# Performance work log

Measured on AMD Instinct MI355X. Metric: run time of the kernel, lower is better.

The kernel has to match this reference:

```python
import jax, jax.numpy as jnp
import numpy as np

TEXTURE_W, SHAPE_W, INTENSITY_W = 1.0, 0.5, 1.0
EPS = 1e-08


def _conv2d_same(x, k):
    # x: [B,1,H,W], k: [1,1,3,3], zero padding 1 (SAME)
    return jax.lax.conv_general_dilated(
        x, k, window_strides=(1, 1), padding='SAME',
        dimension_numbers=('NCHW', 'OIHW', 'NCHW'))


def _box_mean(x):
    # mean over 3x3 zero-padded window == F.unfold(k=3,pad=1).mean(dim=1) for C=1
    k = jnp.ones((1, 1, 3, 3), x.dtype) / 9.0
    return _conv2d_same(x, k)


def _local_variance(x):
    # mean((patch - patch_mean)^2) == E[x^2] - E[x]^2 over the padded 3x3 window
    m = _box_mean(x)
    m2 = _box_mean(x * x)
    return m2 - m * m


def _intensity_loss(inp, out, mask):
    ms = mask.sum() + EPS
    im = (inp * mask).sum() / ms
    om = (out * mask).sum() / ms
    di, do = inp - im, out - om
    iv = (di * di * mask).sum() / ms
    ov = (do * do * mask).sum() / ms
    isk = (di ** 3 * mask).sum() / (ms * (iv ** 1.5 + EPS))
    osk = (do ** 3 * mask).sum() / (ms * (ov ** 1.5 + EPS))
    iku = (di ** 4 * mask).sum() / (ms * (iv ** 2 + EPS))
    oku = (do ** 4 * mask).sum() / (ms * (ov ** 2 + EPS))
    return (im - om) ** 2 + (iv - ov) ** 2 + (isk - osk) ** 2 + (iku - oku) ** 2


def _texture_loss(inp, out, mask):
    it = _local_variance(inp)
    ot = _local_variance(out)
    return jnp.abs(ot * mask - it * mask).mean()


def _shape_loss(inp, out, mask):
    lap = jnp.array([[0., 1., 0.], [1., -4., 1.], [0., 1., 0.]], inp.dtype).reshape(1, 1, 3, 3)
    il = _conv2d_same(inp, lap)
    ol = _conv2d_same(out, lap)
    return jnp.abs(ol * mask - il * mask).mean()


def setup_inputs() -> dict:
    key = jax.random.key(0)
    k1, k2, k3 = jax.random.split(key, 3)
    shape = (32, 1, 512, 512)
    return {
        'input_img': jax.random.normal(k1, shape, jnp.float32),
        'output_img': jax.random.normal(k2, shape, jnp.float32),
        'roi_mask': jax.random.uniform(k3, shape, jnp.float32),
    }


def reference(input_img, output_img, roi_mask):
    intensity = _intensity_loss(input_img, output_img, roi_mask)
    texture = _texture_loss(input_img, output_img, roi_mask)
    shape = _shape_loss(input_img, output_img, roi_mask)
    total = INTENSITY_W * intensity + TEXTURE_W * texture + SHAPE_W * shape
    # stacked [intensity, texture, shape, total] (dict values in original order)
    return jnp.stack([intensity, texture, shape, total])
```

## Files before the change

kernel.cpp:

```cpp
#include <hip/hip_runtime.h>
#include <math.h>

#define H 512
#define W 512
#define BAND 4
#define NQ 11

__device__ __forceinline__ float2 shfl_up1_f2(float2 v, int lane) {
    float2 r;
    r.x = __shfl_up(v.x, 1);
    r.y = __shfl_up(v.y, 1);
    if (lane == 0) { r.x = 0.0f; r.y = 0.0f; }
    return r;
}
__device__ __forceinline__ float2 shfl_dn1_f2(float2 v, int lane) {
    float2 r;
    r.x = __shfl_down(v.x, 1);
    r.y = __shfl_down(v.y, 1);
    if (lane == 63) { r.x = 0.0f; r.y = 0.0f; }
    return r;
}

__device__ __forceinline__ float2 pk_add(float2 a, float2 b) { return make_float2(a.x + b.x, a.y + b.y); }
__device__ __forceinline__ float2 pk_sub(float2 a, float2 b) { return make_float2(a.x - b.x, a.y - b.y); }
__device__ __forceinline__ float2 pk_mul(float2 a, float2 b) { return make_float2(a.x * b.x, a.y * b.y); }
__device__ __forceinline__ float2 pk_muls(float2 a, float s) { return make_float2(a.x * s, a.y * s); }
__device__ __forceinline__ float2 pk_fma(float2 a, float2 b, float2 c) {
    return make_float2(fmaf(a.x, b.x, c.x), fmaf(a.y, b.y, c.y));
}

__device__ __forceinline__ void load_row_pk(const float* __restrict__ inp,
                                            const float* __restrict__ outp,
                                            size_t off, int y, int x0, float2* dst) {
    if (y < 0 || y >= H) {
        #pragma unroll
        for (int j = 0; j < 8; j++) dst[j] = make_float2(0.0f, 0.0f);
    } else {
        const float4* pi = reinterpret_cast<const float4*>(inp  + off + (size_t)y * W + x0);
        const float4* po = reinterpret_cast<const float4*>(outp + off + (size_t)y * W + x0);
        float4 a = pi[0], b = pi[1];
        float4 c = po[0], d = po[1];
        dst[0] = make_float2(a.x, c.x); dst[1] = make_float2(a.y, c.y);
        dst[2] = make_float2(a.z, c.z); dst[3] = make_float2(a.w, c.w);
        dst[4] = make_float2(b.x, d.x); dst[5] = make_float2(b.y, d.y);
        dst[6] = make_float2(b.z, d.z); dst[7] = make_float2(b.w, d.w);
    }
}

__device__ __forceinline__ void load_mask_row(const float* __restrict__ mask, size_t off,
                                              int y, int x0, float* dst) {
    const float4* p = reinterpret_cast<const float4*>(mask + off + (size_t)y * W + x0);
    float4 a = p[0];
    float4 b = p[1];
    dst[0] = a.x; dst[1] = a.y; dst[2] = a.z; dst[3] = a.w;
    dst[4] = b.x; dst[5] = b.y; dst[6] = b.z; dst[7] = b.w;
}

__global__ __launch_bounds__(256) void radiomics_main(
    const float* __restrict__ inp, const float* __restrict__ outp,
    const float* __restrict__ mask, double* __restrict__ partials)
{
    const int tid = threadIdx.x;
    const int lane = tid & 63;
    const int wib = tid >> 6;
    const int gwave = blockIdx.x * 4 + wib;
    const int b = gwave >> 7;
    const int band = gwave & 127;
    const int y0 = band * BAND;
    const size_t off = (size_t)b * H * W;
    const int x0 = lane * 8;

    float2 P[8], C[8], N[8];
    float  Mk[8];

    load_row_pk(inp, outp, off, y0 - 1, x0, P);
    load_row_pk(inp, outp, off, y0,     x0, C);
    load_row_pk(inp, outp, off, y0 + 1, x0, N);
    load_mask_row(mask, off, y0, x0, Mk);

    float  acc0 = 0.0f, accT = 0.0f, accS = 0.0f;
    float2 am1 = make_float2(0,0), am2 = make_float2(0,0);
    float2 am3 = make_float2(0,0), am4 = make_float2(0,0);

    const float inv9 = 1.0f / 9.0f;

    #pragma unroll
    for (int i = 0; i < BAND; i++) {
        if (i) {
            #pragma unroll
            for (int j = 0; j < 8; j++) { P[j] = C[j]; C[j] = N[j]; }
            load_row_pk(inp, outp, off, y0 + i + 1, x0, N);
            load_mask_row(mask, off, y0 + i, x0, Mk);
        }

        float2 s1[8], s2[8];
        #pragma unroll
        for (int j = 0; j < 8; j++) {
            s1[j] = pk_add(pk_add(P[j], C[j]), N[j]);
            s2[j] = pk_fma(P[j], P[j], pk_fma(C[j], C[j], pk_mul(N[j], N[j])));
        }
        float2 h1l = shfl_up1_f2(s1[7], lane), h1r = shfl_dn1_f2(s1[0], lane);
        float2 h2l = shfl_up1_f2(s2[7], lane), h2r = shfl_dn1_f2(s2[0], lane);
        float2 hcl = shfl_up1_f2(C[7],  lane), hcr = shfl_dn1_f2(C[0],  lane);

        #pragma unroll
        for (int j = 0; j < 8; j++) {
            float2 l1 = (j == 0) ? h1l : s1[j-1];
            float2 r1 = (j == 7) ? h1r : s1[j+1];
            float2 l2 = (j == 0) ? h2l : s2[j-1];
            float2 r2 = (j == 7) ? h2r : s2[j+1];
            float2 mn = pk_muls(pk_add(pk_add(l1, s1[j]), r1), inv9);
            float2 e2 = pk_muls(pk_add(pk_add(l2, s2[j]), r2), inv9);
            float2 tv = pk_fma(make_float2(-mn.x, -mn.y), mn, e2);
            float2 cl = (j == 0) ? hcl : C[j-1];
            float2 cr = (j == 7) ? hcr : C[j+1];
            float2 lp = pk_sub(pk_add(pk_add(pk_sub(s1[j], C[j]), cl), cr),
                               pk_muls(C[j], 4.0f));
            float m = Mk[j];
            accT += fabsf(tv.y * m - tv.x * m);
            accS += fabsf(lp.y * m - lp.x * m);
            acc0 += m;
            float2 X = C[j];
            float2 t = pk_muls(X, m);
            am1 = pk_add(am1, t); t = pk_mul(t, X);
            am2 = pk_add(am2, t); t = pk_mul(t, X);
            am3 = pk_add(am3, t); t = pk_mul(t, X);
            am4 = pk_add(am4, t);
        }
    }

    float acc[NQ] = { acc0, am1.x, am2.x, am3.x, am4.x,
                            am1.y, am2.y, am3.y, am4.y, accT, accS };
    #pragma unroll
    for (int q = 0; q < NQ; q++) {
        float v = acc[q];
        #pragma unroll
        for (int o = 32; o > 0; o >>= 1) v += __shfl_down(v, o);
        acc[q] = v;
    }
    __shared__ double red[4][NQ];
    if (lane == 0) {
        #pragma unroll
        for (int q = 0; q < NQ; q++) red[wib][q] = (double)acc[q];
    }
    __syncthreads();
    if (tid < NQ) {
        double s = red[0][tid] + red[1][tid] + red[2][tid] + red[3][tid];
        partials[(size_t)blockIdx.x * NQ + tid] = s;
    }
}

__global__ __launch_bounds__(256) void radiomics_final(
    const double* __restrict__ partials, int nblk, float* __restrict__ out4, double inv_n)
{
    const int tid = threadIdx.x;
    const int lane = tid & 63;
    const int w = tid >> 6;
    double q[NQ];
    #pragma unroll
    for (int k = 0; k < NQ; k++) q[k] = 0.0;
    for (int i = tid; i < nblk; i += 256) {
        #pragma unroll
        for (int k = 0; k < NQ; k++) q[k] += partials[(size_t)i * NQ + k];
    }
    #pragma unroll
    for (int k = 0; k < NQ; k++) {
        #pragma unroll
        for (int o = 32; o > 0; o >>= 1) q[k] += __shfl_down(q[k], o);
    }
    __shared__ double red[4][NQ];
    if (lane == 0) {
        #pragma unroll
        for (int k = 0; k < NQ; k++) red[w][k] = q[k];
    }
    __syncthreads();
    if (tid == 0) {
        double s[NQ];
        #pragma unroll
        for (int k = 0; k < NQ; k++) s[k] = red[0][k] + red[1][k] + red[2][k] + red[3][k];
        const double EPS = 1e-8;
        double S0 = s[0];
        double ms = S0 + EPS;
        double im = s[1] / ms, om = s[5] / ms;
        double im2 = im * im, im3 = im2 * im, im4 = im2 * im2;
        double om2 = om * om, om3 = om2 * om, om4 = om2 * om2;
        double di2 = s[2] - 2.0*im*s[1] + im2*S0;
        double do2 = s[6] - 2.0*om*s[5] + om2*S0;
        double iv = di2 / ms, ov = do2 / ms;
        double di3 = s[3] - 3.0*im*s[2] + 3.0*im2*s[1] - im3*S0;
        double do3 = s[7] - 3.0*om*s[6] + 3.0*om2*s[5] - om3*S0;
        double isk = di3 / (ms * (iv * sqrt(iv) + EPS));
        double osk = do3 / (ms * (ov * sqrt(ov) + EPS));
        double di4 = s[4] - 4.0*im*s[3] + 6.0*im2*s[2] - 4.0*im3*s[1] + im4*S0;
        double do4 = s[8] - 4.0*om*s[7] + 6.0*om2*s[6] - 4.0*om3*s[5] + om4*S0;
        double iku = di4 / (ms * (iv * iv + EPS));
        double oku = do4 / (ms * (ov * ov + EPS));
        double intensity = (im-om)*(im-om) + (iv-ov)*(iv-ov)
                         + (isk-osk)*(isk-osk) + (iku-oku)*(iku-oku);
        double texture = s[9]  * inv_n;
        double shape   = s[10] * inv_n;
        double total = intensity + texture + 0.5 * shape;
        out4[0] = (float)intensity;
        out4[1] = (float)texture;
        out4[2] = (float)shape;
        out4[3] = (float)total;
    }
}

extern "C" void kernel_launch(void* const* d_in, const int* in_sizes, int n_in,
                              void* d_out, int out_size, void* d_ws, size_t ws_size,
                              hipStream_t stream) {
    const float* inp  = (const float*)d_in[0];
    const float* outp = (const float*)d_in[1];
    const float* mask = (const float*)d_in[2];
    const int total = in_sizes[0];
    const int nimg  = total / (H * W);
    const int nwaves = nimg * (H / BAND);
    const int nblk   = nwaves / 4;
    double* partials = (double*)d_ws;

    radiomics_main<<<nblk, 256, 0, stream>>>(inp, outp, mask, partials);
    const double inv_n = 1.0 / (double)total;
    radiomics_final<<<1, 256, 0, stream>>>(partials, nblk, (float*)d_out, inv_n);
}
```

Measured before the change: 124.1 us.

## Fuse final reduction via last-block ticket, double band height, remap blocks across XCDs

Merges the final reduction kernel into the main kernel: each block writes its partials, bumps an atomic ticket, and the last block to finish does the final reduction and writes the four outputs. The band height goes from 4 to 8 rows per wave, which halves the block count and cuts the redundant halo-row loads. Block IDs are remapped so consecutive logical blocks land on the same XCD, aiming for better L2 locality of neighbouring rows. This adds a memset launch for the ticket, a threadfence and an atomic per block, and the tail still has one block doing a serial reduction.

Result: slower. 167.6 us (+35.0%).

```diff
diff --git a/kernel.cpp b/kernel.cpp
--- a/kernel.cpp
+++ b/kernel.cpp
@@ -3,8 +3,9 @@
 
 #define H 512
 #define W 512
-#define BAND 4
+#define BAND 8
 #define NQ 11
+#define CTR_OFF 49152
 
 __device__ __forceinline__ float2 shfl_up1_f2(float2 v, int lane) {
     float2 r;
@@ -56,16 +57,21 @@
     dst[4] = b.x; dst[5] = b.y; dst[6] = b.z; dst[7] = b.w;
 }
 
-__global__ __launch_bounds__(256) void radiomics_main(
+__global__ __launch_bounds__(256) void radiomics_fused(
     const float* __restrict__ inp, const float* __restrict__ outp,
-    const float* __restrict__ mask, double* __restrict__ partials)
+    const float* __restrict__ mask, double* __restrict__ partials,
+    unsigned int* __restrict__ ticket,
+    float* __restrict__ out4, double inv_n, int nblk)
 {
     const int tid = threadIdx.x;
     const int lane = tid & 63;
     const int wib = tid >> 6;
-    const int gwave = blockIdx.x * 4 + wib;
-    const int b = gwave >> 7;
-    const int band = gwave & 127;
+    const int bid = blockIdx.x;
+    const int cpx = nblk >> 3;
+    const int lb = (bid & 7) * cpx + (bid >> 3);
+    const int gwave = lb * 4 + wib;
+    const int b = gwave >> 6;
+    const int band = gwave & 63;
     const int y0 = band * BAND;
     const size_t off = (size_t)b * H * W;
     const int x0 = lane * 8;
@@ -139,6 +145,7 @@
         acc[q] = v;
     }
     __shared__ double red[4][NQ];
+    __shared__ bool isLast;
     if (lane == 0) {
         #pragma unroll
         for (int q = 0; q < NQ; q++) red[wib][q] = (double)acc[q];
@@ -146,16 +153,18 @@
     __syncthreads();
     if (tid < NQ) {
         double s = red[0][tid] + red[1][tid] + red[2][tid] + red[3][tid];
-        partials[(size_t)blockIdx.x * NQ + tid] = s;
-    }
-}
-
-__global__ __launch_bounds__(256) void radiomics_final(
-    const double* __restrict__ partials, int nblk, float* __restrict__ out4, double inv_n)
-{
-    const int tid = threadIdx.x;
-    const int lane = tid & 63;
-    const int w = tid >> 6;
+        partials[(size_t)bid * NQ + tid] = s;
+    }
+    __threadfence();
+    __syncthreads();
+    if (tid == 0) {
+        unsigned int prev = atomicAdd(ticket, 1u);
+        isLast = (prev == (unsigned int)(nblk - 1));
+    }
+    __syncthreads();
+    if (!isLast) return;
+
+    __threadfence();
     double q[NQ];
     #pragma unroll
     for (int k = 0; k < NQ; k++) q[k] = 0.0;
@@ -168,10 +177,10 @@
         #pragma unroll
         for (int o = 32; o > 0; o >>= 1) q[k] += __shfl_down(q[k], o);
     }
-    __shared__ double red[4][NQ];
+    __syncthreads();
     if (lane == 0) {
         #pragma unroll
-        for (int k = 0; k < NQ; k++) red[w][k] = q[k];
+        for (int k = 0; k < NQ; k++) red[wib][k] = q[k];
     }
     __syncthreads();
     if (tid == 0) {
@@ -218,8 +227,11 @@
     const int nwaves = nimg * (H / BAND);
     const int nblk   = nwaves / 4;
     double* partials = (double*)d_ws;
-
-    radiomics_main<<<nblk, 256, 0, stream>>>(inp, outp, mask, partials);
+    unsigned int* ticket = (unsigned int*)((char*)d_ws + CTR_OFF);
+    float* out4 = (float*)d_out;
     const double inv_n = 1.0 / (double)total;
-    radiomics_final<<<1, 256, 0, stream>>>(partials, nblk, (float*)d_out, inv_n);
-}
+
+    hipMemsetAsync((void*)ticket, 0, sizeof(unsigned int), stream);
+    radiomics_fused<<<nblk, 256, 0, stream>>>(inp, outp, mask, partials, ticket,
+                                              out4, inv_n, nblk);
+}
```
